# Kernel tuning notes

Measured on AMD Instinct MI355X. Metric: run time of the kernel, lower is better.

The kernel has to match this reference:

```python
import jax, jax.numpy as jnp
import numpy as np

TAU = 1.0

def _bilinear_sample(lut, coords):
    # lut: (Hl, Wl); coords: (..., 2) with (x, y) in [-1, 1]; align_corners=True,
    # zeros padding for out-of-bounds (matches torch grid_sample defaults).
    Hl, Wl = lut.shape
    x = (coords[..., 0] + 1.0) * 0.5 * (Wl - 1)
    y = (coords[..., 1] + 1.0) * 0.5 * (Hl - 1)
    x0f = jnp.floor(x); y0f = jnp.floor(y)
    wx1 = x - x0f; wx0 = 1.0 - wx1
    wy1 = y - y0f; wy0 = 1.0 - wy1
    ix0 = x0f.astype(jnp.int32); ix1 = ix0 + 1
    iy0 = y0f.astype(jnp.int32); iy1 = iy0 + 1
    def gather(iy, ix):
        valid = (iy >= 0) & (iy < Hl) & (ix >= 0) & (ix < Wl)
        v = lut[jnp.clip(iy, 0, Hl - 1), jnp.clip(ix, 0, Wl - 1)]
        return jnp.where(valid, v, jnp.zeros((), lut.dtype))
    return (gather(iy0, ix0) * (wy0 * wx0) + gather(iy0, ix1) * (wy0 * wx1)
            + gather(iy1, ix0) * (wy1 * wx0) + gather(iy1, ix1) * (wy1 * wx1))

# vmap over the K library axis: lut (K,Hl,Wl), coords (B,K,Ho,Wo,2) -> (B,K,Ho,Wo)
_sample_per_lib = jax.vmap(_bilinear_sample, in_axes=(0, 1), out_axes=1)

def setup_inputs() -> dict:
    key = jax.random.key(0)
    k1, k2, k3, k4, k5 = jax.random.split(key, 5)
    B, K, Ho, Wo = 4, 8, 768, 768
    Hl, Wl = 256, 256
    grid = jax.random.uniform(k1, (B, 2 * K, Ho, Wo), jnp.float32, minval=-1.0, maxval=1.0)
    class_logits = jax.random.normal(k2, (B, K, Ho, Wo), jnp.float32)
    lut0 = jax.random.normal(k3, (K, Hl, Wl), jnp.float32)
    lut1 = jax.random.normal(k4, (K, Hl, Wl), jnp.float32)
    lut2 = jax.random.normal(k5, (K, Hl, Wl), jnp.float32)
    return {"grid": grid, "class_logits": class_logits,
            "lut0": lut0, "lut1": lut1, "lut2": lut2}

def reference(grid, class_logits, lut0, lut1, lut2):
    B, C, Ho, Wo = grid.shape
    K = class_logits.shape[1]
    # (B,2K,H,W) -> (B,K,2,H,W) -> (B,K,H,W,2) with last dim (x,y)
    coords = grid.reshape(B, K, 2, Ho, Wo).transpose(0, 1, 3, 4, 2)
    # soft class weights (use_hard=False): softmax over K with temperature tau
    weights = jax.nn.softmax(class_logits / TAU, axis=1)  # (B,K,Ho,Wo)
    outs = []
    for lut in (lut0, lut1, lut2):
        samp = _sample_per_lib(lut, coords)              # (B,K,Ho,Wo)
        out = jnp.sum(weights * samp, axis=1)[:, None]   # (B,1,Ho,Wo)
        outs.append(out)
    return tuple(outs)
```

## Files before the change

### kernel.cpp

```cpp
#include <hip/hip_runtime.h>
#include <hip/hip_fp16.h>

#define BB 4
#define KK 8
#define HO 768
#define WO 768
#define HWP (HO * WO)
#define NPIX (BB * HWP)
#define NTEX (KK * 256 * 256)

#define QLO   (-6.5f)
#define QSTEP (13.0f / 255.0f)
#define QRCP  (255.0f / 13.0f)

#define TPB 1024
#define PPT 9
#define PIX_PER_BLOCK (TPB * PPT)
#define NBLK (NPIX / PIX_PER_BLOCK)
#define BANDROWS 129
#define BAND_TEXELS (BANDROWS * 256)
#define LDS_BYTES (BAND_TEXELS * 4)

__device__ __forceinline__ unsigned q8(float v) {
    float q = (v - QLO) * QRCP;
    q = fminf(fmaxf(q, 0.0f), 255.0f);
    return (unsigned)(int)rintf(q);
}

__global__ __launch_bounds__(256) void pack_lut_q8_kernel(
    const float* __restrict__ lut0,
    const float* __restrict__ lut1,
    const float* __restrict__ lut2,
    unsigned* __restrict__ dst)
{
    int i = blockIdx.x * blockDim.x + threadIdx.x;
    if (i < NTEX) {
        dst[i] = q8(lut0[i]) | (q8(lut1[i]) << 8) | (q8(lut2[i]) << 16);
    }
}

__device__ __forceinline__ void dec(unsigned t, float w,
                                    float& S0, float& S1, float& S2) {
    S0 = fmaf(w, (float)( t        & 255u), S0);
    S1 = fmaf(w, (float)((t >>  8) & 255u), S1);
    S2 = fmaf(w, (float)((t >> 16) & 255u), S2);
}

__global__ __launch_bounds__(TPB) void keyed_lut_sampler_lds_kernel(
    const float* __restrict__ grid,
    const float* __restrict__ logits,
    const unsigned* __restrict__ lutQ4,
    float* __restrict__ out)
{
    extern __shared__ unsigned ldsu[];

    const int tid = threadIdx.x;
    const int bl  = blockIdx.x;
    const int b   = bl >> 6;
    const int p0  = (bl & 63) * PIX_PER_BLOCK + tid;

    const float* lgb = logits + (size_t)b * KK * HWP;
    const float* grb = grid   + (size_t)b * 2 * KK * HWP;

    float vs[PPT];
    #pragma unroll
    for (int i = 0; i < PPT; ++i) {
        const float* lp = lgb + p0 + i * TPB;
        float ss = 0.f;
        #pragma unroll
        for (int k = 0; k < KK; ++k) {
            ss += __expf(lp[(size_t)k * HWP]);
        }
        vs[i] = 1.0f / ss;
    }

    float S0[PPT], S1[PPT], S2[PPT];
    #pragma unroll
    for (int i = 0; i < PPT; ++i) { S0[i] = 0.f; S1[i] = 0.f; S2[i] = 0.f; }

    #pragma unroll 1
    for (int k = 0; k < KK; ++k) {
        __half2 wAB[PPT], wCD[PPT];
        int ad[PPT];
        #pragma unroll
        for (int i = 0; i < PPT; ++i) {
            const int hw = p0 + i * TPB;
            const float lg = lgb[(size_t)k * HWP + hw];
            const float w  = __expf(lg) * vs[i];
            const float x = __builtin_nontemporal_load(grb + (size_t)(2 * k) * HWP + hw);
            const float y = __builtin_nontemporal_load(grb + (size_t)(2 * k + 1) * HWP + hw);
            const float fx = fmaf(x, 127.5f, 127.5f);
            const float fy = fmaf(y, 127.5f, 127.5f);
            const float x0f = floorf(fx), y0f = floorf(fy);
            const float wx1 = fx - x0f, wy1 = fy - y0f;
            const float wx0 = 1.0f - wx1, wy0 = 1.0f - wy1;
            const int ix0 = min(max((int)x0f, 0), 254);
            const int iy0 = min(max((int)y0f, 0), 254);
            const float a = w * wy0, c = w * wy1;
            wAB[i] = __floats2half2_rn(a * wx0, a * wx1);
            wCD[i] = __floats2half2_rn(c * wx0, c * wx1);
            ad[i] = (iy0 << 8) | ix0;
        }

        const int kbase = k << 16;
        #pragma unroll
        for (int s = 0; s < 2; ++s) {
            __syncthreads();
            {
                const int r0 = s * 127;
                const uint4* src4 = reinterpret_cast<const uint4*>(lutQ4);
                uint4* dst4 = reinterpret_cast<uint4*>(ldsu);
                #pragma unroll
                for (int j = 0; j < 9; ++j) {
                    const int e = tid + j * TPB;
                    if (e < BAND_TEXELS / 4) {
                        const int t   = e * 4;
                        const int gr  = r0 + (t >> 8);
                        const int col = t & 255;
                        dst4[e] = src4[(kbase + (gr << 8) + col) >> 2];
                    }
                }
            }
            __syncthreads();
            const int rofs = s * 127 * 256;
            #pragma unroll
            for (int i = 0; i < PPT; ++i) {
                const int a = ad[i];
                if ((a >> 15) == s) {
                    const int li = a - rofs;
                    const unsigned t00 = ldsu[li];
                    const unsigned t01 = ldsu[li + 1];
                    const unsigned t10 = ldsu[li + 256];
                    const unsigned t11 = ldsu[li + 257];
                    const float2 fab = __half22float2(wAB[i]);
                    const float2 fcd = __half22float2(wCD[i]);
                    dec(t00, fab.x, S0[i], S1[i], S2[i]);
                    dec(t01, fab.y, S0[i], S1[i], S2[i]);
                    dec(t10, fcd.x, S0[i], S1[i], S2[i]);
                    dec(t11, fcd.y, S0[i], S1[i], S2[i]);
                }
            }
        }
    }

    #pragma unroll
    for (int i = 0; i < PPT; ++i) {
        const int idx = b * HWP + p0 + i * TPB;
        __builtin_nontemporal_store(fmaf(S0[i], QSTEP, QLO), out + idx);
        __builtin_nontemporal_store(fmaf(S1[i], QSTEP, QLO), out + NPIX + idx);
        __builtin_nontemporal_store(fmaf(S2[i], QSTEP, QLO), out + 2 * NPIX + idx);
    }
}

extern "C" void kernel_launch(void* const* d_in, const int* in_sizes, int n_in,
                              void* d_out, int out_size, void* d_ws, size_t ws_size,
                              hipStream_t stream) {
    const float* grid   = (const float*)d_in[0];
    const float* logits = (const float*)d_in[1];
    const float* lut0   = (const float*)d_in[2];
    const float* lut1   = (const float*)d_in[3];
    const float* lut2   = (const float*)d_in[4];
    float* out = (float*)d_out;

    unsigned* lutQ4 = (unsigned*)d_ws;

    (void)hipFuncSetAttribute(
        reinterpret_cast<const void*>(keyed_lut_sampler_lds_kernel),
        hipFuncAttributeMaxDynamicSharedMemorySize, LDS_BYTES);

    pack_lut_q8_kernel<<<NTEX / 256, 256, 0, stream>>>(lut0, lut1, lut2, lutQ4);
    keyed_lut_sampler_lds_kernel<<<NBLK, TPB, LDS_BYTES, stream>>>(
        grid, logits, lutQ4, out);
}
```

Baseline: 146.3 us.

## Stage full byte-plane LUTs in LDS with double-buffered prefetch per library

```diff
diff --git a/kernel.cpp b/kernel.cpp
--- a/kernel.cpp
+++ b/kernel.cpp
@@ -1,5 +1,4 @@
 #include <hip/hip_runtime.h>
-#include <hip/hip_fp16.h>
 
 #define BB 4
 #define KK 8
@@ -7,7 +6,8 @@
 #define WO 768
 #define HWP (HO * WO)
 #define NPIX (BB * HWP)
-#define NTEX (KK * 256 * 256)
+#define PLANE 65536
+#define NPLANE 24
 
 #define QLO   (-6.5f)
 #define QSTEP (13.0f / 255.0f)
@@ -17,9 +17,7 @@
 #define PPT 9
 #define PIX_PER_BLOCK (TPB * PPT)
 #define NBLK (NPIX / PIX_PER_BLOCK)
-#define BANDROWS 129
-#define BAND_TEXELS (BANDROWS * 256)
-#define LDS_BYTES (BAND_TEXELS * 4)
+#define LDS_BYTES (2 * PLANE)
 
 __device__ __forceinline__ unsigned q8(float v) {
     float q = (v - QLO) * QRCP;
@@ -27,33 +25,27 @@
     return (unsigned)(int)rintf(q);
 }
 
-__global__ __launch_bounds__(256) void pack_lut_q8_kernel(
+__global__ __launch_bounds__(256) void pack_planes_kernel(
     const float* __restrict__ lut0,
     const float* __restrict__ lut1,
     const float* __restrict__ lut2,
-    unsigned* __restrict__ dst)
+    unsigned char* __restrict__ dst)
 {
-    int i = blockIdx.x * blockDim.x + threadIdx.x;
-    if (i < NTEX) {
-        dst[i] = q8(lut0[i]) | (q8(lut1[i]) << 8) | (q8(lut2[i]) << 16);
+    int i = blockIdx.x * 256 + threadIdx.x;
+    if (i < KK * PLANE) {
+        dst[i]                  = (unsigned char)q8(lut0[i]);
+        dst[i + KK * PLANE]     = (unsigned char)q8(lut1[i]);
+        dst[i + 2 * KK * PLANE] = (unsigned char)q8(lut2[i]);
     }
 }
 
-__device__ __forceinline__ void dec(unsigned t, float w,
-                                    float& S0, float& S1, float& S2) {
-    S0 = fmaf(w, (float)( t        & 255u), S0);
-    S1 = fmaf(w, (float)((t >>  8) & 255u), S1);
-    S2 = fmaf(w, (float)((t >> 16) & 255u), S2);
-}
-
-__global__ __launch_bounds__(TPB) void keyed_lut_sampler_lds_kernel(
+__global__ __launch_bounds__(TPB) void sampler_planes_kernel(
     const float* __restrict__ grid,
     const float* __restrict__ logits,
-    const unsigned* __restrict__ lutQ4,
+    const unsigned char* __restrict__ planes,
     float* __restrict__ out)
 {
-    extern __shared__ unsigned ldsu[];
-
+    extern __shared__ unsigned char lds[];
     const int tid = threadIdx.x;
     const int bl  = blockIdx.x;
     const int b   = bl >> 6;
@@ -68,87 +60,80 @@
         const float* lp = lgb + p0 + i * TPB;
         float ss = 0.f;
         #pragma unroll
-        for (int k = 0; k < KK; ++k) {
-            ss += __expf(lp[(size_t)k * HWP]);
-        }
+        for (int k = 0; k < KK; ++k) ss += __expf(lp[(size_t)k * HWP]);
         vs[i] = 1.0f / ss;
     }
 
-    float S0[PPT], S1[PPT], S2[PPT];
+    float S[3][PPT];
     #pragma unroll
-    for (int i = 0; i < PPT; ++i) { S0[i] = 0.f; S1[i] = 0.f; S2[i] = 0.f; }
+    for (int c = 0; c < 3; ++c) {
+        #pragma unroll
+        for (int i = 0; i < PPT; ++i) S[c][i] = 0.f;
+    }
 
-    #pragma unroll 1
-    for (int k = 0; k < KK; ++k) {
-        __half2 wAB[PPT], wCD[PPT];
-        int ad[PPT];
+    {
+        const uint4* s4 = reinterpret_cast<const uint4*>(planes);
+        uint4* d4 = reinterpret_cast<uint4*>(lds);
         #pragma unroll
-        for (int i = 0; i < PPT; ++i) {
-            const int hw = p0 + i * TPB;
-            const float lg = lgb[(size_t)k * HWP + hw];
-            const float w  = __expf(lg) * vs[i];
-            const float x = __builtin_nontemporal_load(grb + (size_t)(2 * k) * HWP + hw);
-            const float y = __builtin_nontemporal_load(grb + (size_t)(2 * k + 1) * HWP + hw);
-            const float fx = fmaf(x, 127.5f, 127.5f);
-            const float fy = fmaf(y, 127.5f, 127.5f);
-            const float x0f = floorf(fx), y0f = floorf(fy);
-            const float wx1 = fx - x0f, wy1 = fy - y0f;
-            const float wx0 = 1.0f - wx1, wy0 = 1.0f - wy1;
-            const int ix0 = min(max((int)x0f, 0), 254);
-            const int iy0 = min(max((int)y0f, 0), 254);
-            const float a = w * wy0, c = w * wy1;
-            wAB[i] = __floats2half2_rn(a * wx0, a * wx1);
-            wCD[i] = __floats2half2_rn(c * wx0, c * wx1);
-            ad[i] = (iy0 << 8) | ix0;
-        }
+        for (int q = 0; q < 4; ++q) d4[tid + q * TPB] = s4[tid + q * TPB];
+    }
+    __syncthreads();
 
-        const int kbase = k << 16;
-        #pragma unroll
-        for (int s = 0; s < 2; ++s) {
-            __syncthreads();
-            {
-                const int r0 = s * 127;
-                const uint4* src4 = reinterpret_cast<const uint4*>(lutQ4);
-                uint4* dst4 = reinterpret_cast<uint4*>(ldsu);
+    #pragma unroll
+    for (int bank = 0; bank < 3; ++bank) {
+        #pragma unroll 1
+        for (int kk = 0; kk < KK; ++kk) {
+            const int j = bank * KK + kk;
+
+            uint4 tmp[4];
+            if (j + 1 < NPLANE) {
+                const uint4* s4 = reinterpret_cast<const uint4*>(
+                    planes + (size_t)(j + 1) * PLANE);
                 #pragma unroll
-                for (int j = 0; j < 9; ++j) {
-                    const int e = tid + j * TPB;
-                    if (e < BAND_TEXELS / 4) {
-                        const int t   = e * 4;
-                        const int gr  = r0 + (t >> 8);
-                        const int col = t & 255;
-                        dst4[e] = src4[(kbase + (gr << 8) + col) >> 2];
-                    }
-                }
+                for (int q = 0; q < 4; ++q) tmp[q] = s4[tid + q * TPB];
+            }
+
+            const unsigned char* P = lds + (j & 1) * PLANE;
+            #pragma unroll
+            for (int i = 0; i < PPT; ++i) {
+                const int hw = p0 + i * TPB;
+                const float w = __expf(lgb[(size_t)kk * HWP + hw]) * vs[i];
+                const float x = grb[(size_t)(2 * kk) * HWP + hw];
+                const float y = grb[(size_t)(2 * kk + 1) * HWP + hw];
+                const float fx = fmaf(x, 127.5f, 127.5f);
+                const float fy = fmaf(y, 127.5f, 127.5f);
+                const float x0f = floorf(fx), y0f = floorf(fy);
+                const float wx1 = fx - x0f, wy1 = fy - y0f;
+                const float wx0 = 1.0f - wx1, wy0 = 1.0f - wy1;
+                const int ix0 = min(max((int)x0f, 0), 254);
+                const int iy0 = min(max((int)y0f, 0), 254);
+                const int li = (iy0 << 8) | ix0;
+                const float a = w * wy0, c = w * wy1;
+                const float t00 = (float)P[li];
+                const float t01 = (float)P[li + 1];
+                const float t10 = (float)P[li + 256];
+                const float t11 = (float)P[li + 257];
+                S[bank][i] = fmaf(a * wx0, t00,
+                             fmaf(a * wx1, t01,
+                             fmaf(c * wx0, t10,
+                             fmaf(c * wx1, t11, S[bank][i]))));
+            }
+
+            if (j + 1 < NPLANE) {
+                uint4* d4 = reinterpret_cast<uint4*>(lds + ((j + 1) & 1) * PLANE);
+                #pragma unroll
+                for (int q = 0; q < 4; ++q) d4[tid + q * TPB] = tmp[q];
             }
             __syncthreads();
-            const int rofs = s * 127 * 256;
-            #pragma unroll
-            for (int i = 0; i < PPT; ++i) {
-                const int a = ad[i];
-                if ((a >> 15) == s) {
-                    const int li = a - rofs;
-                    const unsigned t00 = ldsu[li];
-                    const unsigned t01 = ldsu[li + 1];
-                    const unsigned t10 = ldsu[li + 256];
-                    const unsigned t11 = ldsu[li + 257];
-                    const float2 fab = __half22float2(wAB[i]);
-                    const float2 fcd = __half22float2(wCD[i]);
-                    dec(t00, fab.x, S0[i], S1[i], S2[i]);
-                    dec(t01, fab.y, S0[i], S1[i], S2[i]);
-                    dec(t10, fcd.x, S0[i], S1[i], S2[i]);
-                    dec(t11, fcd.y, S0[i], S1[i], S2[i]);
-                }
-            }
         }
     }
 
     #pragma unroll
     for (int i = 0; i < PPT; ++i) {
         const int idx = b * HWP + p0 + i * TPB;
-        __builtin_nontemporal_store(fmaf(S0[i], QSTEP, QLO), out + idx);
-        __builtin_nontemporal_store(fmaf(S1[i], QSTEP, QLO), out + NPIX + idx);
-        __builtin_nontemporal_store(fmaf(S2[i], QSTEP, QLO), out + 2 * NPIX + idx);
+        __builtin_nontemporal_store(fmaf(S[0][i], QSTEP, QLO), out + idx);
+        __builtin_nontemporal_store(fmaf(S[1][i], QSTEP, QLO), out + NPIX + idx);
+        __builtin_nontemporal_store(fmaf(S[2][i], QSTEP, QLO), out + 2 * NPIX + idx);
     }
 }
 
@@ -162,13 +147,12 @@
     const float* lut2   = (const float*)d_in[4];
     float* out = (float*)d_out;
 
-    unsigned* lutQ4 = (unsigned*)d_ws;
+    unsigned char* planes = (unsigned char*)d_ws;
 
     (void)hipFuncSetAttribute(
-        reinterpret_cast<const void*>(keyed_lut_sampler_lds_kernel),
+        reinterpret_cast<const void*>(sampler_planes_kernel),
         hipFuncAttributeMaxDynamicSharedMemorySize, LDS_BYTES);
 
-    pack_lut_q8_kernel<<<NTEX / 256, 256, 0, stream>>>(lut0, lut1, lut2, lutQ4);
-    keyed_lut_sampler_lds_kernel<<<NBLK, TPB, LDS_BYTES, stream>>>(
-        grid, logits, lutQ4, out);
+    pack_planes_kernel<<<(KK * PLANE) / 256, 256, 0, stream>>>(lut0, lut1, lut2, planes);
+    sampler_planes_kernel<<<NBLK, TPB, LDS_BYTES, stream>>>(grid, logits, planes, out);
 }
```

Result: slower. 344.9 us (+135.7%).
